# Optimization experiments

Measured on AMD Instinct MI355X. Metric: run time of the kernel, lower is better.

The kernel has to match this reference:

```python
import jax, jax.numpy as jnp
import numpy as np

ALPHA = 0.2  # LeakyReLU negative slope
NEG_INF = -9e15


def setup_inputs() -> dict:
    key = jax.random.key(0)
    k_h, k_adj, k_W, k_a = jax.random.split(key, 4)
    B, N, Din, Dout = 8, 1024, 256, 256
    h = jax.random.normal(k_h, (B, N, Din), dtype=jnp.float32)
    adj = jax.random.randint(k_adj, (B, N, N), 0, 2, dtype=jnp.int32)
    # nn.Linear weight [out, in], xavier-uniform-ish init for a
    W = jax.random.normal(k_W, (Dout, Din), dtype=jnp.float32) * (1.0 / np.sqrt(Din))
    lim = np.float32(1.414 * np.sqrt(6.0 / (2 * Dout + 1)))
    a = jax.random.uniform(k_a, (2 * Dout, 1), dtype=jnp.float32, minval=-lim, maxval=lim)
    return {"h": h, "adj": adj, "W": W, "a": a}


def reference(h, adj, W, a):
    # Wh: [B, N, F]
    Wh = jnp.einsum('bnd,fd->bnf', h, W)
    F_ = Wh.shape[-1]
    # Decompose concat-then-matmul: e_ij = leakyrelu(Wh_i @ a1 + Wh_j @ a2)
    a1 = a[:F_, 0]   # [F]
    a2 = a[F_:, 0]   # [F]
    src = Wh @ a1    # [B, N]  score contribution of row node i
    dst = Wh @ a2    # [B, N]  score contribution of col node j
    e = src[:, :, None] + dst[:, None, :]          # [B, N, N]
    e = jnp.where(e > 0, e, ALPHA * e)             # LeakyReLU
    e = jnp.where(adj > 0, e, NEG_INF)             # mask non-edges
    attention = jax.nn.softmax(e, axis=-1)         # [B, N, N]
    # dropout p=0.0 -> identity in eval/train
    h_prime = jnp.einsum('bij,bjf->bif', attention, Wh)
    return h_prime
```

## Files before the change

kernel.cpp:

```cpp
#include <hip/hip_runtime.h>
#include <hip/hip_bf16.h>
#include <cstdint>

#define ALPHA 0.2f
#define NEG_INF -9000000000000000.0f

typedef __bf16 bf16_t;
typedef __bf16 bf16x8 __attribute__((ext_vector_type(8)));
typedef float f32x16 __attribute__((ext_vector_type(16)));

__global__ __launch_bounds__(256) void k_zero(float* __restrict__ p) {
  *(float4*)(p + (size_t)blockIdx.x * 1024 + threadIdx.x * 4) = make_float4(0.f, 0.f, 0.f, 0.f);
}

__global__ __launch_bounds__(256) void k_gemm1(
    const float* __restrict__ h, const float* __restrict__ W, const float* __restrict__ a,
    bf16_t* __restrict__ WhT, float* __restrict__ src, float* __restrict__ dst)
{
  __shared__ float smem[64 * 68];
  float* As = smem;
  float* Bs = smem + 32 * 68;
  const int m0 = blockIdx.x * 64;
  const int f0 = blockIdx.y * 64;
  const int tid = threadIdx.x;
  const int tm = tid >> 4, tf = tid & 15;
  float acc[4][4] = {};
  for (int k0 = 0; k0 < 256; k0 += 32) {
#pragma unroll
    for (int l = 0; l < 2; l++) {
      int idx = tid + l * 256;
      int r = idx >> 3;
      int c = (idx & 7) << 2;
      float4 va = *(const float4*)(h + (size_t)(m0 + r) * 256 + k0 + c);
      As[(c + 0) * 68 + r] = va.x; As[(c + 1) * 68 + r] = va.y;
      As[(c + 2) * 68 + r] = va.z; As[(c + 3) * 68 + r] = va.w;
      float4 vb = *(const float4*)(W + (size_t)(f0 + r) * 256 + k0 + c);
      Bs[(c + 0) * 68 + r] = vb.x; Bs[(c + 1) * 68 + r] = vb.y;
      Bs[(c + 2) * 68 + r] = vb.z; Bs[(c + 3) * 68 + r] = vb.w;
    }
    __syncthreads();
#pragma unroll
    for (int k = 0; k < 32; k++) {
      float av[4], bv[4];
      *(float4*)av = *(const float4*)&As[k * 68 + tm * 4];
      *(float4*)bv = *(const float4*)&Bs[k * 68 + tf * 4];
#pragma unroll
      for (int i = 0; i < 4; i++)
#pragma unroll
        for (int j = 0; j < 4; j++)
          acc[i][j] = fmaf(av[i], bv[j], acc[i][j]);
    }
    __syncthreads();
  }

#pragma unroll
  for (int i = 0; i < 4; i++)
    *(float4*)&smem[(tm * 4 + i) * 68 + tf * 4] =
        make_float4(acc[i][0], acc[i][1], acc[i][2], acc[i][3]);
  __syncthreads();
  {
    const int fl = tid >> 2;
    const int jq = (tid & 3) * 16;
    const int b  = m0 >> 10;
    const int j0 = m0 & 1023;
    bf16x8 v0, v1;
#pragma unroll
    for (int k = 0; k < 8; k++) {
      v0[k] = (bf16_t)smem[(jq + k) * 68 + fl];
      v1[k] = (bf16_t)smem[(jq + 8 + k) * 68 + fl];
    }
    bf16_t* dp = WhT + (((size_t)(b * 256 + f0 + fl)) << 10) + j0 + jq;
    *(bf16x8*)dp = v0;
    *(bf16x8*)(dp + 8) = v1;
  }
  {
    float a1v[4], a2v[4];
#pragma unroll
    for (int j = 0; j < 4; j++) {
      a1v[j] = a[f0 + tf * 4 + j];
      a2v[j] = a[256 + f0 + tf * 4 + j];
    }
#pragma unroll
    for (int i = 0; i < 4; i++) {
      float s1 = 0.f, s2 = 0.f;
#pragma unroll
      for (int j = 0; j < 4; j++) {
        s1 = fmaf(acc[i][j], a1v[j], s1);
        s2 = fmaf(acc[i][j], a2v[j], s2);
      }
#pragma unroll
      for (int off = 8; off; off >>= 1) {
        s1 += __shfl_down(s1, off, 16);
        s2 += __shfl_down(s2, off, 16);
      }
      if (tf == 0) {
        atomicAdd(&src[m0 + tm * 4 + i], s1);
        atomicAdd(&dst[m0 + tm * 4 + i], s2);
      }
    }
  }
}

__global__ __launch_bounds__(256) void k_stats(
    const int* __restrict__ adj, const float* __restrict__ src, const float* __restrict__ dst,
    float* __restrict__ m_ws, float* __restrict__ linv_ws,
    unsigned long long* __restrict__ mask_ws)
{
  const int b  = blockIdx.x & 7;
  const int i0 = (blockIdx.x >> 3) << 3;
  const int t  = threadIdx.x;
  const int wv = t >> 6, lane = t & 63;
  __shared__ float dstS[1024];
  __shared__ float srcS[8];
  __shared__ float partM[8][4], partL[8][4];
  *(float4*)&dstS[t * 4] = *(const float4*)(dst + (b << 10) + t * 4);
  if (t < 8) srcS[t] = src[(b << 10) + i0 + t];
  __syncthreads();

  for (int i = 0; i < 8; i++) {
    float si = srcS[i];
    const int* arow = adj + (((size_t)(b << 10) + i0 + i) << 10);
    float e4[4];
#pragma unroll
    for (int k = 0; k < 4; k++) {
      int j = k * 256 + t;
      int av = arow[j];
      float v = si + dstS[j];
      float vl = fmaxf(v, ALPHA * v);
      e4[k] = (av > 0) ? vl : NEG_INF;
      unsigned long long bm = __ballot(av > 0);
      if (lane == 0) mask_ws[((size_t)(b << 10) + i0 + i) * 16 + k * 4 + wv] = bm;
    }
    float mt = fmaxf(fmaxf(e4[0], e4[1]), fmaxf(e4[2], e4[3]));
    float lt = __expf(e4[0] - mt) + __expf(e4[1] - mt) +
               __expf(e4[2] - mt) + __expf(e4[3] - mt);
#pragma unroll
    for (int off = 32; off; off >>= 1) {
      float m2 = __shfl_down(mt, off, 64);
      float l2 = __shfl_down(lt, off, 64);
      float nm = fmaxf(mt, m2);
      lt = lt * __expf(mt - nm) + l2 * __expf(m2 - nm);
      mt = nm;
    }
    if (lane == 0) { partM[i][wv] = mt; partL[i][wv] = lt; }
  }
  __syncthreads();
  if (t < 8) {
    float M = fmaxf(fmaxf(partM[t][0], partM[t][1]), fmaxf(partM[t][2], partM[t][3]));
    float L = partL[t][0] * __expf(partM[t][0] - M) + partL[t][1] * __expf(partM[t][1] - M) +
              partL[t][2] * __expf(partM[t][2] - M) + partL[t][3] * __expf(partM[t][3] - M);
    m_ws[(b << 10) + i0 + t] = M;
    linv_ws[(b << 10) + i0 + t] = 1.0f / L;
  }
}

__global__ __launch_bounds__(256) void k_attn(
    const bf16_t* __restrict__ WhT, const float* __restrict__ src, const float* __restrict__ dst,
    const float* __restrict__ m_ws, const float* __restrict__ linv_ws,
    const unsigned long long* __restrict__ mask_ws, float* __restrict__ out)
{
  const int b  = blockIdx.x & 7;
  const int fh = (blockIdx.x >> 3) & 1;
  const int i0 = (blockIdx.x >> 4) << 5;
  const int t  = threadIdx.x;
  const int w  = t >> 6;
  const int lane = t & 63;
  const int mrow = lane & 31, half = lane >> 5;

  __shared__ float dstS[1024];
  __shared__ float srcS[32], mS[32], lInvS[32];
  __shared__ unsigned long long maskS[32 * 16];
  __shared__ bf16_t P[32 * 264];
  __shared__ bf16_t WhS[128 * 72];

  *(float4*)&dstS[t * 4] = *(const float4*)(dst + (b << 10) + t * 4);
  if (t < 32) {
    srcS[t]  = src[(b << 10) + i0 + t];
    mS[t]    = m_ws[(b << 10) + i0 + t];
    lInvS[t] = linv_ws[(b << 10) + i0 + t];
  }
  {
    const size_t mb = ((size_t)(b << 10) + i0) * 16;
    maskS[t]       = mask_ws[mb + t];
    maskS[t + 256] = mask_ws[mb + t + 256];
  }
  __syncthreads();

  f32x16 acc;
#pragma unroll
  for (int r = 0; r < 16; r++) acc[r] = 0.f;

  const size_t whbase = ((size_t)(b * 256 + fh * 128)) << 10;

  for (int c = 0; c < 4; c++) {
    {
      float dj = dstS[c * 256 + t];
      int mi = c * 4 + (t >> 6);
      int sh = t & 63;
#pragma unroll 8
      for (int i = 0; i < 32; i++) {
        unsigned long long w64 = maskS[i * 16 + mi];
        float v = srcS[i] + dj;
        float vl = fmaxf(v, ALPHA * v);
        float e = ((w64 >> sh) & 1ull) ? vl : NEG_INF;
        P[i * 264 + t] = (bf16_t)__expf(e - mS[i]);
      }
    }
    __syncthreads();

    for (int s = 0; s < 4; s++) {
      const size_t gbase = whbase + c * 256 + s * 64;
#pragma unroll
      for (int it = 0; it < 4; it++) {
        int idx = it * 256 + t;
        int f  = idx >> 3;
        int jb = (idx & 7) << 3;
        uint4 v = *(const uint4*)(WhT + gbase + ((size_t)f << 10) + jb);
        *(uint4*)&WhS[f * 72 + jb] = v;
      }
      __syncthreads();
#pragma unroll
      for (int ks = 0; ks < 4; ks++) {
        bf16x8 af = *(const bf16x8*)&P[mrow * 264 + s * 64 + ks * 16 + half * 8];
        bf16x8 bf = *(const bf16x8*)&WhS[(w * 32 + mrow) * 72 + ks * 16 + half * 8];
        acc = __builtin_amdgcn_mfma_f32_32x32x16_bf16(af, bf, acc, 0, 0, 0);
      }
      __syncthreads();
    }
  }

  const int col = fh * 128 + w * 32 + mrow;
#pragma unroll
  for (int r = 0; r < 16; r++) {
    int row = (r & 3) + 8 * (r >> 2) + 4 * half;
    out[((size_t)(b << 10) + i0 + row) * 256 + col] = acc[r] * lInvS[row];
  }
}

extern "C" void kernel_launch(void* const* d_in, const int* in_sizes, int n_in,
                              void* d_out, int out_size, void* d_ws, size_t ws_size,
                              hipStream_t stream) {
  const float* h   = (const float*)d_in[0];
  const int*   adj = (const int*)d_in[1];
  const float* W   = (const float*)d_in[2];
  const float* a   = (const float*)d_in[3];
  float* out = (float*)d_out;

  char* wsb = (char*)d_ws;
  bf16_t* WhT = (bf16_t*)wsb;
  float* srcv = (float*)(wsb + (4u << 20));
  float* dstv = srcv + 8192;
  float* m_ws = srcv + 16384;
  float* linv = srcv + 24576;
  unsigned long long* mask_ws = (unsigned long long*)(wsb + (4u << 20) + 131072);

  k_zero<<<16, 256, 0, stream>>>(srcv);
  k_gemm1<<<dim3(128, 4), 256, 0, stream>>>(h, W, a, WhT, srcv, dstv);
  k_stats<<<1024, 256, 0, stream>>>(adj, srcv, dstv, m_ws, linv, mask_ws);
  k_attn<<<512, 256, 0, stream>>>(WhT, srcv, dstv, m_ws, linv, mask_ws, out);
}
```

Baseline: 136.4 us.

## Use MFMA for projection GEMM, precompute W^T a for scores, vectorize adj loads

Replaces the FP32 FMA projection GEMM with a bf16 MFMA kernel that converts h and W to bf16 on load. The src/dst scores are now computed as h·(Wᵀa), using a tiny prep kernel plus a separate reduction kernel, which removes the atomics and the zeroing kernel. The stats kernel loads adj as int4 per thread and writes the ballot masks in a new bit layout, and the attention kernel's mask indexing is changed to match. This trades fewer GEMM flops and atomics for bf16 rounding of the projection inputs and two extra small launches.

```diff
diff --git a/kernel.cpp b/kernel.cpp
--- a/kernel.cpp
+++ b/kernel.cpp
@@ -9,96 +9,118 @@
 typedef __bf16 bf16x8 __attribute__((ext_vector_type(8)));
 typedef float f32x16 __attribute__((ext_vector_type(16)));
 
-__global__ __launch_bounds__(256) void k_zero(float* __restrict__ p) {
-  *(float4*)(p + (size_t)blockIdx.x * 1024 + threadIdx.x * 4) = make_float4(0.f, 0.f, 0.f, 0.f);
+__global__ __launch_bounds__(256) void k_prep(
+    const float* __restrict__ W, const float* __restrict__ a, float* __restrict__ u)
+{
+  const int d = threadIdx.x;
+  float s1a = 0.f, s1b = 0.f, s2a = 0.f, s2b = 0.f;
+#pragma unroll 4
+  for (int f = 0; f < 256; f += 2) {
+    float w0 = W[f * 256 + d];
+    float w1 = W[(f + 1) * 256 + d];
+    s1a = fmaf(w0, a[f], s1a);       s1b = fmaf(w1, a[f + 1], s1b);
+    s2a = fmaf(w0, a[256 + f], s2a); s2b = fmaf(w1, a[256 + f + 1], s2b);
+  }
+  u[d] = s1a + s1b;
+  u[256 + d] = s2a + s2b;
 }
 
 __global__ __launch_bounds__(256) void k_gemm1(
-    const float* __restrict__ h, const float* __restrict__ W, const float* __restrict__ a,
-    bf16_t* __restrict__ WhT, float* __restrict__ src, float* __restrict__ dst)
-{
-  __shared__ float smem[64 * 68];
-  float* As = smem;
-  float* Bs = smem + 32 * 68;
-  const int m0 = blockIdx.x * 64;
-  const int f0 = blockIdx.y * 64;
-  const int tid = threadIdx.x;
-  const int tm = tid >> 4, tf = tid & 15;
-  float acc[4][4] = {};
-  for (int k0 = 0; k0 < 256; k0 += 32) {
-#pragma unroll
-    for (int l = 0; l < 2; l++) {
-      int idx = tid + l * 256;
-      int r = idx >> 3;
-      int c = (idx & 7) << 2;
-      float4 va = *(const float4*)(h + (size_t)(m0 + r) * 256 + k0 + c);
-      As[(c + 0) * 68 + r] = va.x; As[(c + 1) * 68 + r] = va.y;
-      As[(c + 2) * 68 + r] = va.z; As[(c + 3) * 68 + r] = va.w;
-      float4 vb = *(const float4*)(W + (size_t)(f0 + r) * 256 + k0 + c);
-      Bs[(c + 0) * 68 + r] = vb.x; Bs[(c + 1) * 68 + r] = vb.y;
-      Bs[(c + 2) * 68 + r] = vb.z; Bs[(c + 3) * 68 + r] = vb.w;
+    const float* __restrict__ h, const float* __restrict__ W, bf16_t* __restrict__ WhT)
+{
+  __shared__ bf16_t WS[64 * 72];
+  __shared__ bf16_t HS[64 * 72];
+  const int bx = blockIdx.x;
+  const int b  = bx & 7;
+  const int jt = (bx >> 3) & 15;
+  const int ft = bx >> 7;
+  const int j0 = jt * 64, f0 = ft * 64;
+  const int t = threadIdx.x;
+  const int w = t >> 6, lane = t & 63;
+  const int mrow = lane & 31, half = lane >> 5;
+  const int fsub = (w & 1) * 32, jsub = (w >> 1) * 32;
+
+  const int lr = t >> 2;
+  const int lc = (t & 3) * 16;
+  const float* wp = W + ((size_t)(f0 + lr)) * 256 + lc;
+  const float* hp = h + ((size_t)(b * 1024 + j0 + lr)) * 256 + lc;
+
+  f32x16 acc;
+#pragma unroll
+  for (int r = 0; r < 16; r++) acc[r] = 0.f;
+
+  for (int s = 0; s < 4; s++) {
+    if (s) __syncthreads();
+    {
+      float4 w0 = *(const float4*)(wp + s * 64);
+      float4 w1 = *(const float4*)(wp + s * 64 + 4);
+      float4 w2 = *(const float4*)(wp + s * 64 + 8);
+      float4 w3 = *(const float4*)(wp + s * 64 + 12);
+      bf16x8 va, vb;
+      va[0] = (bf16_t)w0.x; va[1] = (bf16_t)w0.y; va[2] = (bf16_t)w0.z; va[3] = (bf16_t)w0.w;
+      va[4] = (bf16_t)w1.x; va[5] = (bf16_t)w1.y; va[6] = (bf16_t)w1.z; va[7] = (bf16_t)w1.w;
+      vb[0] = (bf16_t)w2.x; vb[1] = (bf16_t)w2.y; vb[2] = (bf16_t)w2.z; vb[3] = (bf16_t)w2.w;
+      vb[4] = (bf16_t)w3.x; vb[5] = (bf16_t)w3.y; vb[6] = (bf16_t)w3.z; vb[7] = (bf16_t)w3.w;
+      *(bf16x8*)&WS[lr * 72 + lc] = va;
+      *(bf16x8*)&WS[lr * 72 + lc + 8] = vb;
+      float4 h0 = *(const float4*)(hp + s * 64);
+      float4 h1 = *(const float4*)(hp + s * 64 + 4);
+      float4 h2 = *(const float4*)(hp + s * 64 + 8);
+      float4 h3 = *(const float4*)(hp + s * 64 + 12);
+      bf16x8 vc, vd;
+      vc[0] = (bf16_t)h0.x; vc[1] = (bf16_t)h0.y; vc[2] = (bf16_t)h0.z; vc[3] = (bf16_t)h0.w;
+      vc[4] = (bf16_t)h1.x; vc[5] = (bf16_t)h1.y; vc[6] = (bf16_t)h1.z; vc[7] = (bf16_t)h1.w;
+      vd[0] = (bf16_t)h2.x; vd[1] = (bf16_t)h2.y; vd[2] = (bf16_t)h2.z; vd[3] = (bf16_t)h2.w;
+      vd[4] = (bf16_t)h3.x; vd[5] = (bf16_t)h3.y; vd[6] = (bf16_t)h3.z; vd[7] = (bf16_t)h3.w;
+      *(bf16x8*)&HS[lr * 72 + lc] = vc;
+      *(bf16x8*)&HS[lr * 72 + lc + 8] = vd;
     }
     __syncthreads();
 #pragma unroll
-    for (int k = 0; k < 32; k++) {
-      float av[4], bv[4];
-      *(float4*)av = *(const float4*)&As[k * 68 + tm * 4];
-      *(float4*)bv = *(const float4*)&Bs[k * 68 + tf * 4];
-#pragma unroll
-      for (int i = 0; i < 4; i++)
-#pragma unroll
-        for (int j = 0; j < 4; j++)
-          acc[i][j] = fmaf(av[i], bv[j], acc[i][j]);
-    }
-    __syncthreads();
-  }
-
-#pragma unroll
-  for (int i = 0; i < 4; i++)
-    *(float4*)&smem[(tm * 4 + i) * 68 + tf * 4] =
-        make_float4(acc[i][0], acc[i][1], acc[i][2], acc[i][3]);
-  __syncthreads();
-  {
-    const int fl = tid >> 2;
-    const int jq = (tid & 3) * 16;
-    const int b  = m0 >> 10;
-    const int j0 = m0 & 1023;
-    bf16x8 v0, v1;
-#pragma unroll
-    for (int k = 0; k < 8; k++) {
-      v0[k] = (bf16_t)smem[(jq + k) * 68 + fl];
-      v1[k] = (bf16_t)smem[(jq + 8 + k) * 68 + fl];
-    }
-    bf16_t* dp = WhT + (((size_t)(b * 256 + f0 + fl)) << 10) + j0 + jq;
-    *(bf16x8*)dp = v0;
-    *(bf16x8*)(dp + 8) = v1;
-  }
-  {
-    float a1v[4], a2v[4];
-#pragma unroll
-    for (int j = 0; j < 4; j++) {
-      a1v[j] = a[f0 + tf * 4 + j];
-      a2v[j] = a[256 + f0 + tf * 4 + j];
-    }
-#pragma unroll
-    for (int i = 0; i < 4; i++) {
-      float s1 = 0.f, s2 = 0.f;
-#pragma unroll
-      for (int j = 0; j < 4; j++) {
-        s1 = fmaf(acc[i][j], a1v[j], s1);
-        s2 = fmaf(acc[i][j], a2v[j], s2);
-      }
-#pragma unroll
-      for (int off = 8; off; off >>= 1) {
-        s1 += __shfl_down(s1, off, 16);
-        s2 += __shfl_down(s2, off, 16);
-      }
-      if (tf == 0) {
-        atomicAdd(&src[m0 + tm * 4 + i], s1);
-        atomicAdd(&dst[m0 + tm * 4 + i], s2);
-      }
-    }
-  }
+    for (int ks = 0; ks < 4; ks++) {
+      bf16x8 af = *(const bf16x8*)&WS[(fsub + mrow) * 72 + ks * 16 + half * 8];
+      bf16x8 bf = *(const bf16x8*)&HS[(jsub + mrow) * 72 + ks * 16 + half * 8];
+      acc = __builtin_amdgcn_mfma_f32_32x32x16_bf16(af, bf, acc, 0, 0, 0);
+    }
+  }
+
+  const int jcol = j0 + jsub + mrow;
+#pragma unroll
+  for (int r = 0; r < 16; r++) {
+    int frow = fsub + (r & 3) + 8 * (r >> 2) + 4 * half;
+    WhT[(((size_t)(b * 256 + f0 + frow)) << 10) + jcol] = (bf16_t)acc[r];
+  }
+}
+
+__global__ __launch_bounds__(256) void k_src(
+    const float* __restrict__ h, const float* __restrict__ u,
+    float* __restrict__ src, float* __restrict__ dst)
+{
+  __shared__ float uS[512];
+  const int t = threadIdx.x;
+  uS[t] = u[t];
+  uS[256 + t] = u[256 + t];
+  __syncthreads();
+  const int n = t >> 4, c = t & 15;
+  const int m = blockIdx.x * 16 + n;
+  const float* hp = h + (size_t)m * 256 + c * 16;
+  float s1 = 0.f, s2 = 0.f;
+#pragma unroll
+  for (int i = 0; i < 4; i++) {
+    float4 v = *(const float4*)(hp + i * 4);
+    const float* u1p = &uS[c * 16 + i * 4];
+    const float* u2p = &uS[256 + c * 16 + i * 4];
+    s1 = fmaf(v.x, u1p[0], s1); s1 = fmaf(v.y, u1p[1], s1);
+    s1 = fmaf(v.z, u1p[2], s1); s1 = fmaf(v.w, u1p[3], s1);
+    s2 = fmaf(v.x, u2p[0], s2); s2 = fmaf(v.y, u2p[1], s2);
+    s2 = fmaf(v.z, u2p[2], s2); s2 = fmaf(v.w, u2p[3], s2);
+  }
+#pragma unroll
+  for (int off = 8; off; off >>= 1) {
+    s1 += __shfl_down(s1, off, 16);
+    s2 += __shfl_down(s2, off, 16);
+  }
+  if (c == 0) { src[m] = s1; dst[m] = s2; }
 }
 
 __global__ __launch_bounds__(256) void k_stats(
@@ -119,17 +141,24 @@
 
   for (int i = 0; i < 8; i++) {
     float si = srcS[i];
-    const int* arow = adj + (((size_t)(b << 10) + i0 + i) << 10);
+    const size_t row = (size_t)(b << 10) + i0 + i;
+    const int4 av = *(const int4*)(adj + (row << 10) + 4 * t);
+    float4 dj = *(const float4*)&dstS[4 * t];
     float e4[4];
-#pragma unroll
-    for (int k = 0; k < 4; k++) {
-      int j = k * 256 + t;
-      int av = arow[j];
-      float v = si + dstS[j];
-      float vl = fmaxf(v, ALPHA * v);
-      e4[k] = (av > 0) ? vl : NEG_INF;
-      unsigned long long bm = __ballot(av > 0);
-      if (lane == 0) mask_ws[((size_t)(b << 10) + i0 + i) * 16 + k * 4 + wv] = bm;
+    {
+      float v0 = si + dj.x, v1 = si + dj.y, v2 = si + dj.z, v3 = si + dj.w;
+      e4[0] = (av.x > 0) ? fmaxf(v0, ALPHA * v0) : NEG_INF;
+      e4[1] = (av.y > 0) ? fmaxf(v1, ALPHA * v1) : NEG_INF;
+      e4[2] = (av.z > 0) ? fmaxf(v2, ALPHA * v2) : NEG_INF;
+      e4[3] = (av.w > 0) ? fmaxf(v3, ALPHA * v3) : NEG_INF;
+    }
+    unsigned long long b0 = __ballot(av.x > 0);
+    unsigned long long b1 = __ballot(av.y > 0);
+    unsigned long long b2 = __ballot(av.z > 0);
+    unsigned long long b3 = __ballot(av.w > 0);
+    if (lane == 0) {
+      unsigned long long* mp = mask_ws + row * 16 + wv * 4;
+      mp[0] = b0; mp[1] = b1; mp[2] = b2; mp[3] = b3;
     }
     float mt = fmaxf(fmaxf(e4[0], e4[1]), fmaxf(e4[2], e4[3]));
     float lt = __expf(e4[0] - mt) + __expf(e4[1] - mt) +
@@ -195,8 +224,8 @@
   for (int c = 0; c < 4; c++) {
     {
       float dj = dstS[c * 256 + t];
-      int mi = c * 4 + (t >> 6);
-      int sh = t & 63;
+      int mi = c * 4 + (t & 3);
+      int sh = t >> 2;
 #pragma unroll 8
       for (int i = 0; i < 32; i++) {
         unsigned long long w64 = maskS[i * 16 + mi];
@@ -253,9 +282,11 @@
   float* m_ws = srcv + 16384;
   float* linv = srcv + 24576;
   unsigned long long* mask_ws = (unsigned long long*)(wsb + (4u << 20) + 131072);
-
-  k_zero<<<16, 256, 0, stream>>>(srcv);
-  k_gemm1<<<dim3(128, 4), 256, 0, stream>>>(h, W, a, WhT, srcv, dstv);
+  float* u_ws = (float*)(wsb + (5u << 20) + 131072);
+
+  k_prep <<<1,    256, 0, stream>>>(W, a, u_ws);
+  k_gemm1<<<512,  256, 0, stream>>>(h, W, WhT);
+  k_src  <<<512,  256, 0, stream>>>(h, u_ws, srcv, dstv);
   k_stats<<<1024, 256, 0, stream>>>(adj, srcv, dstv, m_ws, linv, mask_ws);
-  k_attn<<<512, 256, 0, stream>>>(WhT, srcv, dstv, m_ws, linv, mask_ws, out);
-}
+  k_attn <<<512,  256, 0, stream>>>(WhT, srcv, dstv, m_ws, linv, mask_ws, out);
+}
```

After: 130.9 us. 1.04x faster.
